# Kernel optimization log

Hardware: AMD Instinct MI355X
Metric: run time of the kernel (lower is better)

## Reference

```python
import jax, jax.numpy as jnp
import numpy as np

B, N, D, C, K = 16, 8192, 128, 64, 4
SEQ_LEN, PRED_LEN = 96, 192
BASE_TEMP = 2.0


def setup_inputs() -> dict:
    key = jax.random.key(0)
    kx, kd = jax.random.split(key)
    x = jax.random.normal(kx, (B, N, D), dtype=jnp.float32)
    # nn.Parameter(torch.randn(C, D)) followed by nn.init.orthogonal_ -> orthonormal rows
    dict_raw = jax.random.normal(kd, (C, D), dtype=jnp.float32)
    qmat, _ = jnp.linalg.qr(dict_raw.T)  # (D, C), orthonormal columns since D >= C
    dictionary = qmat.T  # (C, D) with orthonormal rows
    return {"x": x, "dictionary": dictionary}


def reference(x, dictionary):
    # x: (B, N, D); dictionary: (C, D)
    temp = BASE_TEMP * (1.0 + PRED_LEN / SEQ_LEN)  # seq_len/pred_len branch active
    scores = jnp.einsum('bnd,cd->bnc', x, dictionary)  # (B, N, C)

    # soft assignment q and KL self-training loss against target distribution p (no grad through p)
    logq = jax.nn.log_softmax(scores / temp, axis=-1)
    q = jnp.exp(logq)
    q_flat = q.reshape(-1, C)  # (B*N, C)
    w = q_flat ** 2 / q_flat.sum(axis=0)
    p = jax.lax.stop_gradient(w / w.sum(axis=1, keepdims=True))
    # F.kl_div(log q, p, reduction='batchmean') = sum(p * (log p - log q)) / (B*N)
    kl_loss = jnp.sum(p * (jnp.log(p) - logq.reshape(-1, C))) / (B * N)

    # orthogonality regularizer on dictionary gram matrix
    gram = dictionary @ dictionary.T  # (C, C)
    ortho_loss = jnp.mean((gram - jnp.eye(C, dtype=dictionary.dtype)) ** 2)
    aux_loss = kl_loss * (SEQ_LEN / PRED_LEN) + 0.1 * ortho_loss

    # top-k hard routing: masked softmax over top-k scores == softmax over the top-k values
    topk_vals, topk_idx = jax.lax.top_k(scores, K)  # (B, N, K)
    wk = jax.nn.softmax(topk_vals / temp, axis=-1)  # (B, N, K)
    # gather only the K selected dictionary rows instead of dense (B,N,C,D) expand
    x_common = jnp.einsum('bnk,bnkd->bnd', wk, dictionary[topk_idx])
    x_residual = x - x_common
    return (x_common, x_residual, aux_loss)
```

## Files before the change

### kernel.cpp

```cpp
#include <hip/hip_runtime.h>
#include <math.h>

#define BB 16
#define NN 8192
#define DD 128
#define CC 64
#define ROWS (BB*NN)
#define INV_TEMP (1.0f/6.0f)
#define NEGF (-3.402823e38f)
#define LDSS 132

#define RPB 128
#define CHW 32
#define XST 34

__device__ __forceinline__ unsigned f2bf(float f) {
    unsigned u = __builtin_bit_cast(unsigned, f);
    return (u + 0x7fffu + ((u >> 16) & 1u)) >> 16;
}
__device__ __forceinline__ float bflo(unsigned u) { return __builtin_bit_cast(float, u << 16); }
__device__ __forceinline__ float bfhi(unsigned u) { return __builtin_bit_cast(float, u & 0xffff0000u); }

__global__ __launch_bounds__(256, 4) void k_main(
    const float* __restrict__ x, const float* __restrict__ dict,
    float* __restrict__ xcg, float* __restrict__ xrg,
    unsigned* __restrict__ qg, float* __restrict__ colpart)
{
    __shared__ __align__(16) float bufA[RPB * XST];
    __shared__ float red2[RPB][2];
    __shared__ float colsumA[CC];
    __shared__ __align__(16) float w4s[RPB][4];
    __shared__ __align__(16) int   si4s[RPB][4];

    const int tid   = threadIdx.x;
    const int rloc  = tid & (RPB - 1);
    const int chalf = tid >> 7;
    const int cbase = __builtin_amdgcn_readfirstlane(chalf << 5);
    const int row0  = blockIdx.x * RPB;

    if (tid < CC) colsumA[tid] = 0.f;

    const int sr = tid >> 3;
    const int sj = (tid & 7) * 4;
    const float* xstage = x + (size_t)(row0 + sr) * DD + sj;

    float s[32];
#pragma unroll
    for (int cc = 0; cc < 32; ++cc) s[cc] = 0.f;

    float4 rp[4];
#pragma unroll
    for (int p = 0; p < 4; ++p)
        rp[p] = *(const float4*)(xstage + (size_t)p * 32 * DD);
#pragma unroll
    for (int p = 0; p < 4; ++p) {
        float* dst = &bufA[XST * (sr + 32 * p) + sj];
        *(float2*)dst       = make_float2(rp[p].x, rp[p].y);
        *(float2*)(dst + 2) = make_float2(rp[p].z, rp[p].w);
    }
    __syncthreads();

    for (int ch = 0; ch < 4; ++ch) {
        const int j0 = ch * CHW;
        if (ch < 3) {
#pragma unroll
            for (int p = 0; p < 4; ++p)
                rp[p] = *(const float4*)(xstage + (size_t)p * 32 * DD + (j0 + CHW));
        }
        const float* xrow = &bufA[XST * rloc];
        for (int js = 0; js < CHW; js += 4) {
            const float2 x01 = *(const float2*)(xrow + js);
            const float2 x23 = *(const float2*)(xrow + js + 2);
            const float* dcol = dict + (size_t)cbase * DD + (j0 + js);
#pragma unroll
            for (int cc = 0; cc < 32; ++cc) {
                const float* dp = dcol + cc * DD;
                float acc = s[cc];
                acc = fmaf(x01.x, dp[0], acc);
                acc = fmaf(x01.y, dp[1], acc);
                acc = fmaf(x23.x, dp[2], acc);
                acc = fmaf(x23.y, dp[3], acc);
                s[cc] = acc;
            }
        }
        if (ch < 3) {
            __syncthreads();
#pragma unroll
            for (int p = 0; p < 4; ++p) {
                float* dst = &bufA[XST * (sr + 32 * p) + sj];
                *(float2*)dst       = make_float2(rp[p].x, rp[p].y);
                *(float2*)(dst + 2) = make_float2(rp[p].z, rp[p].w);
            }
            __syncthreads();
        }
    }

    float lm = s[0];
#pragma unroll
    for (int cc = 1; cc < 32; ++cc) lm = fmaxf(lm, s[cc]);
    red2[rloc][chalf] = lm;
    __syncthreads();
    const float mg = fmaxf(red2[rloc][0], red2[rloc][1]);
    __syncthreads();

    float tv[4]; int ti[4];
    {
        float best = NEGF; int bi = 0;
#pragma unroll
        for (int cc = 0; cc < 32; ++cc) { if (s[cc] > best) { best = s[cc]; bi = cc; } }
        tv[0] = best; ti[0] = bi;
    }
    {
        float best = NEGF; int bi = 0;
#pragma unroll
        for (int cc = 0; cc < 32; ++cc) {
            const float v = (cc == ti[0]) ? NEGF : s[cc];
            if (v > best) { best = v; bi = cc; }
        }
        tv[1] = best; ti[1] = bi;
    }
    {
        float best = NEGF; int bi = 0;
#pragma unroll
        for (int cc = 0; cc < 32; ++cc) {
            const float v = (cc == ti[0] || cc == ti[1]) ? NEGF : s[cc];
            if (v > best) { best = v; bi = cc; }
        }
        tv[2] = best; ti[2] = bi;
    }
    {
        float best = NEGF; int bi = 0;
#pragma unroll
        for (int cc = 0; cc < 32; ++cc) {
            const float v = (cc == ti[0] || cc == ti[1] || cc == ti[2]) ? NEGF : s[cc];
            if (v > best) { best = v; bi = cc; }
        }
        tv[3] = best; ti[3] = bi;
    }

    float lz = 0.f;
#pragma unroll
    for (int cc = 0; cc < 32; ++cc) {
        const float e = __expf((s[cc] - mg) * INV_TEMP);
        s[cc] = e; lz += e;
    }
    red2[rloc][chalf] = lz;
    __syncthreads();
    const float rZ = 1.f / (red2[rloc][0] + red2[rloc][1]);
#pragma unroll
    for (int cc = 0; cc < 32; ++cc) s[cc] *= rZ;

    float* t4v = bufA;
    int*   t4i = (int*)(bufA + 1024);
    {
        const int b4 = (rloc * 2 + chalf) * 4;
#pragma unroll
        for (int k = 0; k < 4; ++k) { t4v[b4 + k] = tv[k]; t4i[b4 + k] = cbase + ti[k]; }
    }
    __syncthreads();
    float cv[8]; int ci[8];
#pragma unroll
    for (int h = 0; h < 2; ++h) {
#pragma unroll
        for (int k = 0; k < 4; ++k) {
            cv[h * 4 + k] = t4v[(rloc * 2 + h) * 4 + k];
            ci[h * 4 + k] = t4i[(rloc * 2 + h) * 4 + k];
        }
    }
    __syncthreads();

    int rank[8];
#pragma unroll
    for (int j = 0; j < 8; ++j) rank[j] = 0;
#pragma unroll
    for (int j = 0; j < 8; ++j) {
#pragma unroll
        for (int k = 0; k < 8; ++k) {
            if (k == j) continue;
            const bool kg = (cv[k] > cv[j]) || (cv[k] == cv[j] && ci[k] < ci[j]);
            rank[j] += kg ? 1 : 0;
        }
    }
    float sv[4]; int si[4];
#pragma unroll
    for (int t2 = 0; t2 < 4; ++t2) { sv[t2] = NEGF; si[t2] = 0; }
#pragma unroll
    for (int j = 0; j < 8; ++j) {
#pragma unroll
        for (int t2 = 0; t2 < 4; ++t2) {
            const bool sel = (rank[j] == t2);
            sv[t2] = sel ? cv[j] : sv[t2];
            si[t2] = sel ? ci[j] : si[t2];
        }
    }
    const float e1 = __expf((sv[1] - sv[0]) * INV_TEMP);
    const float e2 = __expf((sv[2] - sv[0]) * INV_TEMP);
    const float e3 = __expf((sv[3] - sv[0]) * INV_TEMP);
    const float rZ4 = 1.f / (1.f + e1 + e2 + e3);
    const float w0 = rZ4, w1 = e1 * rZ4, w2 = e2 * rZ4, w3 = e3 * rZ4;

    if (chalf == 0) {
        *(float4*)&w4s[rloc][0] = make_float4(w0, w1, w2, w3);
        *(int4*)&si4s[rloc][0]  = make_int4(si[0], si[1], si[2], si[3]);
    }

    {
        unsigned* qs = (unsigned*)bufA;
        const int base = XST * rloc + 16 * chalf;
#pragma unroll
        for (int k2 = 0; k2 < 16; k2 += 2) {
            uint2 w;
            w.x = (f2bf(s[2 * k2 + 1]) << 16) | f2bf(s[2 * k2 + 0]);
            w.y = (f2bf(s[2 * k2 + 3]) << 16) | f2bf(s[2 * k2 + 2]);
            *(uint2*)&qs[base + k2] = w;
        }
        __syncthreads();
        unsigned* qdst = qg + (size_t)blockIdx.x * (RPB * 32);
#pragma unroll
        for (int k4 = 0; k4 < 4; ++k4) {
            const int gd  = k4 * 1024 + tid * 4;
            const int row = gd >> 5, kk = gd & 31;
            const uint2 a = *(const uint2*)&qs[XST * row + kk];
            const uint2 b = *(const uint2*)&qs[XST * row + kk + 2];
            uint4 o; o.x = a.x; o.y = a.y; o.z = b.x; o.w = b.y;
            *(uint4*)&qdst[gd] = o;
        }
        const int cp  = tid & 31;
        const int rr0 = (tid >> 5) * 16;
        float c0 = 0.f, c1 = 0.f;
#pragma unroll
        for (int rr = 0; rr < 16; ++rr) {
            const unsigned u = qs[XST * (rr0 + rr) + cp];
            c0 += bflo(u); c1 += bfhi(u);
        }
        atomicAdd(&colsumA[2 * cp + 0], c0);
        atomicAdd(&colsumA[2 * cp + 1], c1);
    }
    __syncthreads();
    if (tid < CC) colpart[blockIdx.x * CC + tid] = colsumA[tid];

#pragma unroll 2
    for (int it = 0; it < 16; ++it) {
        const int gd  = it * 1024 + tid * 4;
        const int row = gd >> 7;
        const int dd  = gd & 127;
        const float4 wv = *(const float4*)&w4s[row][0];
        const int4  iv  = *(const int4*)&si4s[row][0];
        const size_t go = (size_t)(row0 + row) * DD + dd;
        const float4 xv = *(const float4*)(x + go);
        const float4 d0 = *(const float4*)(dict + (size_t)iv.x * DD + dd);
        const float4 d1 = *(const float4*)(dict + (size_t)iv.y * DD + dd);
        const float4 d2 = *(const float4*)(dict + (size_t)iv.z * DD + dd);
        const float4 d3 = *(const float4*)(dict + (size_t)iv.w * DD + dd);
        float4 c4, r4;
        c4.x = fmaf(wv.w, d3.x, fmaf(wv.z, d2.x, fmaf(wv.y, d1.x, wv.x * d0.x)));
        c4.y = fmaf(wv.w, d3.y, fmaf(wv.z, d2.y, fmaf(wv.y, d1.y, wv.x * d0.y)));
        c4.z = fmaf(wv.w, d3.z, fmaf(wv.z, d2.z, fmaf(wv.y, d1.z, wv.x * d0.z)));
        c4.w = fmaf(wv.w, d3.w, fmaf(wv.z, d2.w, fmaf(wv.y, d1.w, wv.x * d0.w)));
        r4.x = xv.x - c4.x; r4.y = xv.y - c4.y;
        r4.z = xv.z - c4.z; r4.w = xv.w - c4.w;
        *(float4*)(xcg + go) = c4;
        *(float4*)(xrg + go) = r4;
    }
}

__global__ void k_colsum(const float* __restrict__ colpart, float* __restrict__ colsum)
{
    const int tid = threadIdx.x;
    const int c   = tid & 63;
    const int seg = blockIdx.x * 4 + (tid >> 6);
    float v = 0.f;
#pragma unroll
    for (int b = 0; b < 16; ++b)
        v += colpart[(seg * 16 + b) * 64 + c];
    atomicAdd(&colsum[c], v);
}

__global__ __launch_bounds__(256, 2) void k_kl(
    const unsigned* __restrict__ qg, const float* __restrict__ colsum,
    float* __restrict__ klacc)
{
    __shared__ __align__(8) unsigned qs[256 * XST];
    __shared__ float rF[CC], lF[CC];
    __shared__ float kred[4];
    const int tid = threadIdx.x;
    if (tid < CC) { const float F = colsum[tid]; rF[tid] = 1.f / F; lF[tid] = __logf(F); }
    const unsigned* qb = qg + (size_t)blockIdx.x * 8192;
#pragma unroll
    for (int g = 0; g < 8; ++g) {
        const int gd = g * 1024 + tid * 4;
        const uint4 v = *(const uint4*)(qb + gd);
        const int row = gd >> 5, kk = gd & 31;
        *(uint2*)&qs[XST * row + kk]     = make_uint2(v.x, v.y);
        *(uint2*)&qs[XST * row + kk + 2] = make_uint2(v.z, v.w);
    }
    __syncthreads();
    const unsigned* qr = &qs[XST * tid];
    unsigned u[32];
#pragma unroll
    for (int k = 0; k < 32; k += 2) {
        const uint2 t2 = *(const uint2*)&qr[k];
        u[k] = t2.x; u[k + 1] = t2.y;
    }
    float S = 0.f;
#pragma unroll
    for (int k = 0; k < 32; ++k) {
        const float f0 = bflo(u[k]), f1 = bfhi(u[k]);
        S = fmaf(f0 * f0, rF[2 * k], S);
        S = fmaf(f1 * f1, rF[2 * k + 1], S);
    }
    const float rS = 1.f / S;
    const float lS = __logf(S);
    float acc = 0.f;
#pragma unroll
    for (int k = 0; k < 32; ++k) {
        const float f0 = bflo(u[k]), f1 = bfhi(u[k]);
        const float p0 = f0 * f0 * rF[2 * k] * rS;
        const float p1 = f1 * f1 * rF[2 * k + 1] * rS;
        acc += p0 * (__logf(f0) - lF[2 * k] - lS);
        acc += p1 * (__logf(f1) - lF[2 * k + 1] - lS);
    }
#pragma unroll
    for (int off = 32; off > 0; off >>= 1) acc += __shfl_down(acc, off, 64);
    if ((tid & 63) == 0) kred[tid >> 6] = acc;
    __syncthreads();
    if (tid == 0) atomicAdd(klacc, kred[0] + kred[1] + kred[2] + kred[3]);
}

__global__ __launch_bounds__(256) void k_ortho(
    const float* __restrict__ dict, float* __restrict__ oacc)
{
    __shared__ __align__(16) float dlds[CC * LDSS];
    const int tid = threadIdx.x;
    for (int idx = tid; idx < CC * DD; idx += 256)
        dlds[(idx >> 7) * LDSS + (idx & 127)] = dict[idx];
    __syncthreads();

    const int e = blockIdx.x * 256 + tid;
    const int i = e >> 6, jj = e & 63;
    const float* di = &dlds[i * LDSS];
    const float* dj = &dlds[jj * LDSS];
    float g = 0.f;
#pragma unroll 8
    for (int d = 0; d < DD; d += 4) {
        const float4 a = *(const float4*)(di + d);
        const float4 b = *(const float4*)(dj + d);
        g += a.x * b.x + a.y * b.y + a.z * b.z + a.w * b.w;
    }
    const float diff = g - ((i == jj) ? 1.f : 0.f);
    float v = diff * diff;
#pragma unroll
    for (int off = 32; off > 0; off >>= 1)
        v += __shfl_down(v, off, 64);
    if ((tid & 63) == 0) atomicAdd(oacc, v);
}

__global__ void k_final(const float* __restrict__ klacc,
                        const float* __restrict__ oacc,
                        float* __restrict__ out_scalar)
{
    out_scalar[0] = 0.5f * (klacc[0] / (float)ROWS) + 0.1f * (oacc[0] / 4096.f);
}

extern "C" void kernel_launch(void* const* d_in, const int* in_sizes, int n_in,
                              void* d_out, int out_size, void* d_ws, size_t ws_size,
                              hipStream_t stream)
{
    const float* x    = (const float*)d_in[0];
    const float* dict = (const float*)d_in[1];
    float* out = (float*)d_out;
    float* xcg = out;
    float* xrg = out + (size_t)ROWS * DD;
    float* aux = out + 2 * (size_t)ROWS * DD;

    float* ws      = (float*)d_ws;
    float* colsum  = ws;
    float* klacc   = ws + 64;
    float* oacc    = ws + 65;
    float* colpart = ws + 256;
    unsigned* qbuf = (unsigned*)(ws + 256 + 1024 * 64);

    hipMemsetAsync(d_ws, 0, 1024, stream);

    k_main  <<<ROWS / RPB, 256, 0, stream>>>(x, dict, xcg, xrg, qbuf, colpart);
    k_colsum<<<16,         256, 0, stream>>>(colpart, colsum);
    k_kl    <<<ROWS / 256, 256, 0, stream>>>(qbuf, colsum, klacc);
    k_ortho <<<16,         256, 0, stream>>>(dict, oacc);
    k_final <<<1,          1,   0, stream>>>(klacc, oacc, aux);
}
```

Measured before the change: 276.3 us.

## Fuse pipeline into one cooperative kernel with grid syncs, keep q in registers

Replaces the five-kernel sequence with a single cooperative-launch kernel that uses grid-wide syncs to compute column sums, the ortho loss, the KL loss and the final aux scalar. The soft-assignment probabilities stay in registers instead of being written as bf16 to global memory and reread by a separate KL kernel. Launch overhead and the q round trip go away. In exchange it needs all 1024 blocks co-resident (4 per CU) and pays three grid barriers, and it falls back to the old multi-kernel path if the cooperative launch fails.

```diff
diff --git a/kernel.cpp b/kernel.cpp
--- a/kernel.cpp
+++ b/kernel.cpp
@@ -1,5 +1,8 @@
 #include <hip/hip_runtime.h>
+#include <hip/hip_cooperative_groups.h>
 #include <math.h>
+
+namespace cg = cooperative_groups;
 
 #define BB 16
 #define NN 8192
@@ -21,10 +24,12 @@
 __device__ __forceinline__ float bflo(unsigned u) { return __builtin_bit_cast(float, u << 16); }
 __device__ __forceinline__ float bfhi(unsigned u) { return __builtin_bit_cast(float, u & 0xffff0000u); }
 
-__global__ __launch_bounds__(256, 4) void k_main(
+__global__ __launch_bounds__(256, 4) void k_fused(
     const float* __restrict__ x, const float* __restrict__ dict,
     float* __restrict__ xcg, float* __restrict__ xrg,
-    unsigned* __restrict__ qg, float* __restrict__ colpart)
+    float* __restrict__ colpart, float* __restrict__ colsum,
+    float* __restrict__ klacc, float* __restrict__ oacc,
+    float* __restrict__ aux)
 {
     __shared__ __align__(16) float bufA[RPB * XST];
     __shared__ float red2[RPB][2];
@@ -32,12 +37,16 @@
     __shared__ __align__(16) float w4s[RPB][4];
     __shared__ __align__(16) int   si4s[RPB][4];
 
+    cg::grid_group gg = cg::this_grid();
+
     const int tid   = threadIdx.x;
     const int rloc  = tid & (RPB - 1);
     const int chalf = tid >> 7;
     const int cbase = __builtin_amdgcn_readfirstlane(chalf << 5);
-    const int row0  = blockIdx.x * RPB;
-
+    const int bid   = blockIdx.x;
+    const int row0  = bid * RPB;
+
+    if (bid == 0 && tid == 0) { klacc[0] = 0.f; oacc[0] = 0.f; }
     if (tid < CC) colsumA[tid] = 0.f;
 
     const int sr = tid >> 3;
@@ -215,16 +224,6 @@
             *(uint2*)&qs[base + k2] = w;
         }
         __syncthreads();
-        unsigned* qdst = qg + (size_t)blockIdx.x * (RPB * 32);
-#pragma unroll
-        for (int k4 = 0; k4 < 4; ++k4) {
-            const int gd  = k4 * 1024 + tid * 4;
-            const int row = gd >> 5, kk = gd & 31;
-            const uint2 a = *(const uint2*)&qs[XST * row + kk];
-            const uint2 b = *(const uint2*)&qs[XST * row + kk + 2];
-            uint4 o; o.x = a.x; o.y = a.y; o.z = b.x; o.w = b.y;
-            *(uint4*)&qdst[gd] = o;
-        }
         const int cp  = tid & 31;
         const int rr0 = (tid >> 5) * 16;
         float c0 = 0.f, c1 = 0.f;
@@ -237,7 +236,75 @@
         atomicAdd(&colsumA[2 * cp + 1], c1);
     }
     __syncthreads();
-    if (tid < CC) colpart[blockIdx.x * CC + tid] = colsumA[tid];
+    if (tid < CC) colpart[bid * CC + tid] = colsumA[tid];
+
+    gg.sync();
+
+    if (bid == 0) {
+        const int c = tid & 63, qt = tid >> 6;
+        float v = 0.f;
+#pragma unroll 8
+        for (int i = 0; i < 256; ++i)
+            v += colpart[(size_t)(((qt << 8) + i) * 64 + c)];
+        float* cred = bufA;
+        cred[tid] = v;
+        __syncthreads();
+        if (tid < CC)
+            colsum[tid] = cred[tid] + cred[tid + 64] + cred[tid + 128] + cred[tid + 192];
+    } else if (bid >= 64 && bid < 80) {
+        const int e = (bid - 64) * 256 + tid;
+        const int i = e >> 6, jj = e & 63;
+        const float* di = dict + (size_t)i * DD;
+        const float* dj = dict + (size_t)jj * DD;
+        float g = 0.f;
+#pragma unroll 8
+        for (int d = 0; d < DD; d += 4) {
+            const float4 a = *(const float4*)(di + d);
+            const float4 b = *(const float4*)(dj + d);
+            g += a.x * b.x + a.y * b.y + a.z * b.z + a.w * b.w;
+        }
+        const float diff = g - ((i == jj) ? 1.f : 0.f);
+        float v = diff * diff;
+#pragma unroll
+        for (int off = 32; off > 0; off >>= 1)
+            v += __shfl_down(v, off, 64);
+        if ((tid & 63) == 0) atomicAdd(oacc, v);
+    }
+
+    gg.sync();
+
+    {
+        float* rF   = bufA;
+        float* lF   = bufA + 64;
+        float* kred = bufA + 128;
+        if (tid < CC) { const float F = colsum[tid]; rF[tid] = 1.f / F; lF[tid] = __logf(F); }
+        __syncthreads();
+        float Sh = 0.f;
+#pragma unroll
+        for (int cc = 0; cc < 32; ++cc) Sh = fmaf(s[cc] * s[cc], rF[cbase + cc], Sh);
+        red2[rloc][chalf] = Sh;
+        __syncthreads();
+        const float Sr = red2[rloc][0] + red2[rloc][1];
+        const float rS = 1.f / Sr;
+        const float lS = __logf(Sr);
+        float acc = 0.f;
+#pragma unroll
+        for (int cc = 0; cc < 32; ++cc) {
+            const float q = s[cc];
+            const float p = q * q * rF[cbase + cc] * rS;
+            acc += p * (__logf(q) - lF[cbase + cc] - lS);
+        }
+#pragma unroll
+        for (int off = 32; off > 0; off >>= 1) acc += __shfl_down(acc, off, 64);
+        if ((tid & 63) == 0) kred[tid >> 6] = acc;
+        __syncthreads();
+        if (tid == 0) atomicAdd(klacc, kred[0] + kred[1] + kred[2] + kred[3]);
+    }
+
+    gg.sync();
+
+    if (bid == 0 && tid == 0)
+        aux[0] = 0.5f * (klacc[0] / (float)ROWS) + 0.1f * (oacc[0] / 4096.f);
 
 #pragma unroll 2
     for (int it = 0; it < 16; ++it) {
@@ -264,6 +331,249 @@
     }
 }
 
+__global__ __launch_bounds__(256, 4) void k_main(
+    const float* __restrict__ x, const float* __restrict__ dict,
+    float* __restrict__ xcg, float* __restrict__ xrg,
+    unsigned* __restrict__ qg, float* __restrict__ colpart)
+{
+    __shared__ __align__(16) float bufA[RPB * XST];
+    __shared__ float red2[RPB][2];
+    __shared__ float colsumA[CC];
+    __shared__ __align__(16) float w4s[RPB][4];
+    __shared__ __align__(16) int   si4s[RPB][4];
+
+    const int tid   = threadIdx.x;
+    const int rloc  = tid & (RPB - 1);
+    const int chalf = tid >> 7;
+    const int cbase = __builtin_amdgcn_readfirstlane(chalf << 5);
+    const int row0  = blockIdx.x * RPB;
+
+    if (tid < CC) colsumA[tid] = 0.f;
+
+    const int sr = tid >> 3;
+    const int sj = (tid & 7) * 4;
+    const float* xstage = x + (size_t)(row0 + sr) * DD + sj;
+
+    float s[32];
+#pragma unroll
+    for (int cc = 0; cc < 32; ++cc) s[cc] = 0.f;
+
+    float4 rp[4];
+#pragma unroll
+    for (int p = 0; p < 4; ++p)
+        rp[p] = *(const float4*)(xstage + (size_t)p * 32 * DD);
+#pragma unroll
+    for (int p = 0; p < 4; ++p) {
+        float* dst = &bufA[XST * (sr + 32 * p) + sj];
+        *(float2*)dst       = make_float2(rp[p].x, rp[p].y);
+        *(float2*)(dst + 2) = make_float2(rp[p].z, rp[p].w);
+    }
+    __syncthreads();
+
+    for (int ch = 0; ch < 4; ++ch) {
+        const int j0 = ch * CHW;
+        if (ch < 3) {
+#pragma unroll
+            for (int p = 0; p < 4; ++p)
+                rp[p] = *(const float4*)(xstage + (size_t)p * 32 * DD + (j0 + CHW));
+        }
+        const float* xrow = &bufA[XST * rloc];
+        for (int js = 0; js < CHW; js += 4) {
+            const float2 x01 = *(const float2*)(xrow + js);
+            const float2 x23 = *(const float2*)(xrow + js + 2);
+            const float* dcol = dict + (size_t)cbase * DD + (j0 + js);
+#pragma unroll
+            for (int cc = 0; cc < 32; ++cc) {
+                const float* dp = dcol + cc * DD;
+                float acc = s[cc];
+                acc = fmaf(x01.x, dp[0], acc);
+                acc = fmaf(x01.y, dp[1], acc);
+                acc = fmaf(x23.x, dp[2], acc);
+                acc = fmaf(x23.y, dp[3], acc);
+                s[cc] = acc;
+            }
+        }
+        if (ch < 3) {
+            __syncthreads();
+#pragma unroll
+            for (int p = 0; p < 4; ++p) {
+                float* dst = &bufA[XST * (sr + 32 * p) + sj];
+                *(float2*)dst       = make_float2(rp[p].x, rp[p].y);
+                *(float2*)(dst + 2) = make_float2(rp[p].z, rp[p].w);
+            }
+            __syncthreads();
+        }
+    }
+
+    float lm = s[0];
+#pragma unroll
+    for (int cc = 1; cc < 32; ++cc) lm = fmaxf(lm, s[cc]);
+    red2[rloc][chalf] = lm;
+    __syncthreads();
+    const float mg = fmaxf(red2[rloc][0], red2[rloc][1]);
+    __syncthreads();
+
+    float tv[4]; int ti[4];
+    {
+        float best = NEGF; int bi = 0;
+#pragma unroll
+        for (int cc = 0; cc < 32; ++cc) { if (s[cc] > best) { best = s[cc]; bi = cc; } }
+        tv[0] = best; ti[0] = bi;
+    }
+    {
+        float best = NEGF; int bi = 0;
+#pragma unroll
+        for (int cc = 0; cc < 32; ++cc) {
+            const float v = (cc == ti[0]) ? NEGF : s[cc];
+            if (v > best) { best = v; bi = cc; }
+        }
+        tv[1] = best; ti[1] = bi;
+    }
+    {
+        float best = NEGF; int bi = 0;
+#pragma unroll
+        for (int cc = 0; cc < 32; ++cc) {
+            const float v = (cc == ti[0] || cc == ti[1]) ? NEGF : s[cc];
+            if (v > best) { best = v; bi = cc; }
+        }
+        tv[2] = best; ti[2] = bi;
+    }
+    {
+        float best = NEGF; int bi = 0;
+#pragma unroll
+        for (int cc = 0; cc < 32; ++cc) {
+            const float v = (cc == ti[0] || cc == ti[1] || cc == ti[2]) ? NEGF : s[cc];
+            if (v > best) { best = v; bi = cc; }
+        }
+        tv[3] = best; ti[3] = bi;
+    }
+
+    float lz = 0.f;
+#pragma unroll
+    for (int cc = 0; cc < 32; ++cc) {
+        const float e = __expf((s[cc] - mg) * INV_TEMP);
+        s[cc] = e; lz += e;
+    }
+    red2[rloc][chalf] = lz;
+    __syncthreads();
+    const float rZ = 1.f / (red2[rloc][0] + red2[rloc][1]);
+#pragma unroll
+    for (int cc = 0; cc < 32; ++cc) s[cc] *= rZ;
+
+    float* t4v = bufA;
+    int*   t4i = (int*)(bufA + 1024);
+    {
+        const int b4 = (rloc * 2 + chalf) * 4;
+#pragma unroll
+        for (int k = 0; k < 4; ++k) { t4v[b4 + k] = tv[k]; t4i[b4 + k] = cbase + ti[k]; }
+    }
+    __syncthreads();
+    float cv[8]; int ci[8];
+#pragma unroll
+    for (int h = 0; h < 2; ++h) {
+#pragma unroll
+        for (int k = 0; k < 4; ++k) {
+            cv[h * 4 + k] = t4v[(rloc * 2 + h) * 4 + k];
+            ci[h * 4 + k] = t4i[(rloc * 2 + h) * 4 + k];
+        }
+    }
+    __syncthreads();
+
+    int rank[8];
+#pragma unroll
+    for (int j = 0; j < 8; ++j) rank[j] = 0;
+#pragma unroll
+    for (int j = 0; j < 8; ++j) {
+#pragma unroll
+        for (int k = 0; k < 8; ++k) {
+            if (k == j) continue;
+            const bool kg = (cv[k] > cv[j]) || (cv[k] == cv[j] && ci[k] < ci[j]);
+            rank[j] += kg ? 1 : 0;
+        }
+    }
+    float sv[4]; int si[4];
+#pragma unroll
+    for (int t2 = 0; t2 < 4; ++t2) { sv[t2] = NEGF; si[t2] = 0; }
+#pragma unroll
+    for (int j = 0; j < 8; ++j) {
+#pragma unroll
+        for (int t2 = 0; t2 < 4; ++t2) {
+            const bool sel = (rank[j] == t2);
+            sv[t2] = sel ? cv[j] : sv[t2];
+            si[t2] = sel ? ci[j] : si[t2];
+        }
+    }
+    const float e1 = __expf((sv[1] - sv[0]) * INV_TEMP);
+    const float e2 = __expf((sv[2] - sv[0]) * INV_TEMP);
+    const float e3 = __expf((sv[3] - sv[0]) * INV_TEMP);
+    const float rZ4 = 1.f / (1.f + e1 + e2 + e3);
+    const float w0 = rZ4, w1 = e1 * rZ4, w2 = e2 * rZ4, w3 = e3 * rZ4;
+
+    if (chalf == 0) {
+        *(float4*)&w4s[rloc][0] = make_float4(w0, w1, w2, w3);
+        *(int4*)&si4s[rloc][0]  = make_int4(si[0], si[1], si[2], si[3]);
+    }
+
+    {
+        unsigned* qs = (unsigned*)bufA;
+        const int base = XST * rloc + 16 * chalf;
+#pragma unroll
+        for (int k2 = 0; k2 < 16; k2 += 2) {
+            uint2 w;
+            w.x = (f2bf(s[2 * k2 + 1]) << 16) | f2bf(s[2 * k2 + 0]);
+            w.y = (f2bf(s[2 * k2 + 3]) << 16) | f2bf(s[2 * k2 + 2]);
+            *(uint2*)&qs[base + k2] = w;
+        }
+        __syncthreads();
+        unsigned* qdst = qg + (size_t)blockIdx.x * (RPB * 32);
+#pragma unroll
+        for (int k4 = 0; k4 < 4; ++k4) {
+            const int gd  = k4 * 1024 + tid * 4;
+            const int row = gd >> 5, kk = gd & 31;
+            const uint2 a = *(const uint2*)&qs[XST * row + kk];
+            const uint2 b = *(const uint2*)&qs[XST * row + kk + 2];
+            uint4 o; o.x = a.x; o.y = a.y; o.z = b.x; o.w = b.y;
+            *(uint4*)&qdst[gd] = o;
+        }
+        const int cp  = tid & 31;
+        const int rr0 = (tid >> 5) * 16;
+        float c0 = 0.f, c1 = 0.f;
+#pragma unroll
+        for (int rr = 0; rr < 16; ++rr) {
+            const unsigned u = qs[XST * (rr0 + rr) + cp];
+            c0 += bflo(u); c1 += bfhi(u);
+        }
+        atomicAdd(&colsumA[2 * cp + 0], c0);
+        atomicAdd(&colsumA[2 * cp + 1], c1);
+    }
+    __syncthreads();
+    if (tid < CC) colpart[blockIdx.x * CC + tid] = colsumA[tid];
+
+#pragma unroll 2
+    for (int it = 0; it < 16; ++it) {
+        const int gd  = it * 1024 + tid * 4;
+        const int row = gd >> 7;
+        const int dd  = gd & 127;
+        const float4 wv = *(const float4*)&w4s[row][0];
+        const int4  iv  = *(const int4*)&si4s[row][0];
+        const size_t go = (size_t)(row0 + row) * DD + dd;
+        const float4 xv = *(const float4*)(x + go);
+        const float4 d0 = *(const float4*)(dict + (size_t)iv.x * DD + dd);
+        const float4 d1 = *(const float4*)(dict + (size_t)iv.y * DD + dd);
+        const float4 d2 = *(const float4*)(dict + (size_t)iv.z * DD + dd);
+        const float4 d3 = *(const float4*)(dict + (size_t)iv.w * DD + dd);
+        float4 c4, r4;
+        c4.x = fmaf(wv.w, d3.x, fmaf(wv.z, d2.x, fmaf(wv.y, d1.x, wv.x * d0.x)));
+        c4.y = fmaf(wv.w, d3.y, fmaf(wv.z, d2.y, fmaf(wv.y, d1.y, wv.x * d0.y)));
+        c4.z = fmaf(wv.w, d3.z, fmaf(wv.z, d2.z, fmaf(wv.y, d1.z, wv.x * d0.z)));
+        c4.w = fmaf(wv.w, d3.w, fmaf(wv.z, d2.w, fmaf(wv.y, d1.w, wv.x * d0.w)));
+        r4.x = xv.x - c4.x; r4.y = xv.y - c4.y;
+        r4.z = xv.z - c4.z; r4.w = xv.w - c4.w;
+        *(float4*)(xcg + go) = c4;
+        *(float4*)(xrg + go) = r4;
+    }
+}
+
 __global__ void k_colsum(const float* __restrict__ colpart, float* __restrict__ colsum)
 {
     const int tid = threadIdx.x;
@@ -380,11 +690,26 @@
     float* colpart = ws + 256;
     unsigned* qbuf = (unsigned*)(ws + 256 + 1024 * 64);
 
-    hipMemsetAsync(d_ws, 0, 1024, stream);
-
-    k_main  <<<ROWS / RPB, 256, 0, stream>>>(x, dict, xcg, xrg, qbuf, colpart);
-    k_colsum<<<16,         256, 0, stream>>>(colpart, colsum);
-    k_kl    <<<ROWS / 256, 256, 0, stream>>>(qbuf, colsum, klacc);
-    k_ortho <<<16,         256, 0, stream>>>(dict, oacc);
-    k_final <<<1,          1,   0, stream>>>(klacc, oacc, aux);
+    void* kargs[9];
+    kargs[0] = (void*)&x;
+    kargs[1] = (void*)&dict;
+    kargs[2] = (void*)&xcg;
+    kargs[3] = (void*)&xrg;
+    kargs[4] = (void*)&colpart;
+    kargs[5] = (void*)&colsum;
+    kargs[6] = (void*)&klacc;
+    kargs[7] = (void*)&oacc;
+    kargs[8] = (void*)&aux;
+
+    hipError_t rc = hipLaunchCooperativeKernel((const void*)k_fused,
+                                               dim3(ROWS / RPB), dim3(256),
+                                               kargs, 0, stream);
+    if (rc != hipSuccess) {
+        hipMemsetAsync(d_ws, 0, 1024, stream);
+        k_main  <<<ROWS / RPB, 256, 0, stream>>>(x, dict, xcg, xrg, qbuf, colpart);
+        k_colsum<<<16,         256, 0, stream>>>(colpart, colsum);
+        k_kl    <<<ROWS / 256, 256, 0, stream>>>(qbuf, colsum, klacc);
+        k_ortho <<<16,         256, 0, stream>>>(dict, oacc);
+        k_final <<<1,          1,   0, stream>>>(klacc, oacc, aux);
+    }
 }
```

Result: slower. 527.9 us (+91.1%).

## Fuse all stages into one kernel with a grid-wide flag barrier

Applied to the files above, without the earlier changes.

Merges the colsum, KL, ortho and final kernels into the main kernel. The last block to finish reduces the per-block column partials and raises a flag. Every block spins on that flag after writing its outputs, then computes the KL term from the q values still held in registers. This removes the bf16 q buffer write and re-read and four extra launches, and the ortho work moves onto 16 of the blocks. In exchange it relies on all 1024 blocks being resident at once; if they are not, the spin-wait deadlocks.

```diff
diff --git a/kernel.cpp b/kernel.cpp
--- a/kernel.cpp
+++ b/kernel.cpp
@@ -8,11 +8,11 @@
 #define ROWS (BB*NN)
 #define INV_TEMP (1.0f/6.0f)
 #define NEGF (-3.402823e38f)
-#define LDSS 132
 
 #define RPB 128
 #define CHW 32
 #define XST 34
+#define GRID (ROWS / RPB)
 
 __device__ __forceinline__ unsigned f2bf(float f) {
     unsigned u = __builtin_bit_cast(unsigned, f);
@@ -21,22 +21,27 @@
 __device__ __forceinline__ float bflo(unsigned u) { return __builtin_bit_cast(float, u << 16); }
 __device__ __forceinline__ float bfhi(unsigned u) { return __builtin_bit_cast(float, u & 0xffff0000u); }
 
-__global__ __launch_bounds__(256, 4) void k_main(
+__global__ __launch_bounds__(256, 4) void k_all(
     const float* __restrict__ x, const float* __restrict__ dict,
     float* __restrict__ xcg, float* __restrict__ xrg,
-    unsigned* __restrict__ qg, float* __restrict__ colpart)
+    float* __restrict__ colpart, float* __restrict__ colsum,
+    float* __restrict__ klacc, float* __restrict__ oacc,
+    unsigned* __restrict__ cnt1, unsigned* __restrict__ flag,
+    unsigned* __restrict__ cnt2, float* __restrict__ aux)
 {
     __shared__ __align__(16) float bufA[RPB * XST];
     __shared__ float red2[RPB][2];
     __shared__ float colsumA[CC];
     __shared__ __align__(16) float w4s[RPB][4];
     __shared__ __align__(16) int   si4s[RPB][4];
+    __shared__ int lastA;
 
     const int tid   = threadIdx.x;
     const int rloc  = tid & (RPB - 1);
     const int chalf = tid >> 7;
     const int cbase = __builtin_amdgcn_readfirstlane(chalf << 5);
-    const int row0  = blockIdx.x * RPB;
+    const int bid   = blockIdx.x;
+    const int row0  = bid * RPB;
 
     if (tid < CC) colsumA[tid] = 0.f;
 
@@ -215,16 +220,6 @@
             *(uint2*)&qs[base + k2] = w;
         }
         __syncthreads();
-        unsigned* qdst = qg + (size_t)blockIdx.x * (RPB * 32);
-#pragma unroll
-        for (int k4 = 0; k4 < 4; ++k4) {
-            const int gd  = k4 * 1024 + tid * 4;
-            const int row = gd >> 5, kk = gd & 31;
-            const uint2 a = *(const uint2*)&qs[XST * row + kk];
-            const uint2 b = *(const uint2*)&qs[XST * row + kk + 2];
-            uint4 o; o.x = a.x; o.y = a.y; o.z = b.x; o.w = b.y;
-            *(uint4*)&qdst[gd] = o;
-        }
         const int cp  = tid & 31;
         const int rr0 = (tid >> 5) * 16;
         float c0 = 0.f, c1 = 0.f;
@@ -237,7 +232,52 @@
         atomicAdd(&colsumA[2 * cp + 1], c1);
     }
     __syncthreads();
-    if (tid < CC) colpart[blockIdx.x * CC + tid] = colsumA[tid];
+    if (tid < CC) colpart[bid * CC + tid] = colsumA[tid];
+
+    if (bid >= 64 && bid < 80) {
+        const int e = (bid - 64) * 256 + tid;
+        const int i = e >> 6, jj = e & 63;
+        const float* di = dict + (size_t)i * DD;
+        const float* dj = dict + (size_t)jj * DD;
+        float g = 0.f;
+#pragma unroll 8
+        for (int d = 0; d < DD; d += 4) {
+            const float4 a = *(const float4*)(di + d);
+            const float4 b = *(const float4*)(dj + d);
+            g += a.x * b.x + a.y * b.y + a.z * b.z + a.w * b.w;
+        }
+        const float diff = g - ((i == jj) ? 1.f : 0.f);
+        float v = diff * diff;
+#pragma unroll
+        for (int off = 32; off > 0; off >>= 1)
+            v += __shfl_down(v, off, 64);
+        if ((tid & 63) == 0) atomicAdd(oacc, v);
+    }
+
+    __syncthreads();
+    if (tid == 0) {
+        const unsigned prev = __hip_atomic_fetch_add(
+            cnt1, 1u, __ATOMIC_ACQ_REL, __HIP_MEMORY_SCOPE_AGENT);
+        lastA = (prev == (unsigned)(GRID - 1)) ? 1 : 0;
+    }
+    __syncthreads();
+    if (lastA) {
+        const int c = tid & 63, qt = tid >> 6;
+        float v = 0.f;
+#pragma unroll 8
+        for (int i = 0; i < 256; ++i)
+            v += colpart[(size_t)(((qt << 8) + i) * 64 + c)];
+        float* cred = bufA;
+        cred[tid] = v;
+        __syncthreads();
+        if (tid < CC)
+            __hip_atomic_store(&colsum[tid],
+                cred[tid] + cred[tid + 64] + cred[tid + 128] + cred[tid + 192],
+                __ATOMIC_RELAXED, __HIP_MEMORY_SCOPE_AGENT);
+        __syncthreads();
+        if (tid == 0)
+            __hip_atomic_store(flag, 1u, __ATOMIC_RELEASE, __HIP_MEMORY_SCOPE_AGENT);
+    }
 
 #pragma unroll 2
     for (int it = 0; it < 16; ++it) {
@@ -262,104 +302,55 @@
         *(float4*)(xcg + go) = c4;
         *(float4*)(xrg + go) = r4;
     }
-}
-
-__global__ void k_colsum(const float* __restrict__ colpart, float* __restrict__ colsum)
-{
-    const int tid = threadIdx.x;
-    const int c   = tid & 63;
-    const int seg = blockIdx.x * 4 + (tid >> 6);
-    float v = 0.f;
-#pragma unroll
-    for (int b = 0; b < 16; ++b)
-        v += colpart[(seg * 16 + b) * 64 + c];
-    atomicAdd(&colsum[c], v);
-}
-
-__global__ __launch_bounds__(256, 2) void k_kl(
-    const unsigned* __restrict__ qg, const float* __restrict__ colsum,
-    float* __restrict__ klacc)
-{
-    __shared__ __align__(8) unsigned qs[256 * XST];
-    __shared__ float rF[CC], lF[CC];
-    __shared__ float kred[4];
-    const int tid = threadIdx.x;
-    if (tid < CC) { const float F = colsum[tid]; rF[tid] = 1.f / F; lF[tid] = __logf(F); }
-    const unsigned* qb = qg + (size_t)blockIdx.x * 8192;
-#pragma unroll
-    for (int g = 0; g < 8; ++g) {
-        const int gd = g * 1024 + tid * 4;
-        const uint4 v = *(const uint4*)(qb + gd);
-        const int row = gd >> 5, kk = gd & 31;
-        *(uint2*)&qs[XST * row + kk]     = make_uint2(v.x, v.y);
-        *(uint2*)&qs[XST * row + kk + 2] = make_uint2(v.z, v.w);
-    }
-    __syncthreads();
-    const unsigned* qr = &qs[XST * tid];
-    unsigned u[32];
-#pragma unroll
-    for (int k = 0; k < 32; k += 2) {
-        const uint2 t2 = *(const uint2*)&qr[k];
-        u[k] = t2.x; u[k + 1] = t2.y;
-    }
-    float S = 0.f;
-#pragma unroll
-    for (int k = 0; k < 32; ++k) {
-        const float f0 = bflo(u[k]), f1 = bfhi(u[k]);
-        S = fmaf(f0 * f0, rF[2 * k], S);
-        S = fmaf(f1 * f1, rF[2 * k + 1], S);
-    }
-    const float rS = 1.f / S;
-    const float lS = __logf(S);
-    float acc = 0.f;
-#pragma unroll
-    for (int k = 0; k < 32; ++k) {
-        const float f0 = bflo(u[k]), f1 = bfhi(u[k]);
-        const float p0 = f0 * f0 * rF[2 * k] * rS;
-        const float p1 = f1 * f1 * rF[2 * k + 1] * rS;
-        acc += p0 * (__logf(f0) - lF[2 * k] - lS);
-        acc += p1 * (__logf(f1) - lF[2 * k + 1] - lS);
-    }
-#pragma unroll
-    for (int off = 32; off > 0; off >>= 1) acc += __shfl_down(acc, off, 64);
-    if ((tid & 63) == 0) kred[tid >> 6] = acc;
-    __syncthreads();
-    if (tid == 0) atomicAdd(klacc, kred[0] + kred[1] + kred[2] + kred[3]);
-}
-
-__global__ __launch_bounds__(256) void k_ortho(
-    const float* __restrict__ dict, float* __restrict__ oacc)
-{
-    __shared__ __align__(16) float dlds[CC * LDSS];
-    const int tid = threadIdx.x;
-    for (int idx = tid; idx < CC * DD; idx += 256)
-        dlds[(idx >> 7) * LDSS + (idx & 127)] = dict[idx];
-    __syncthreads();
-
-    const int e = blockIdx.x * 256 + tid;
-    const int i = e >> 6, jj = e & 63;
-    const float* di = &dlds[i * LDSS];
-    const float* dj = &dlds[jj * LDSS];
-    float g = 0.f;
-#pragma unroll 8
-    for (int d = 0; d < DD; d += 4) {
-        const float4 a = *(const float4*)(di + d);
-        const float4 b = *(const float4*)(dj + d);
-        g += a.x * b.x + a.y * b.y + a.z * b.z + a.w * b.w;
-    }
-    const float diff = g - ((i == jj) ? 1.f : 0.f);
-    float v = diff * diff;
-#pragma unroll
-    for (int off = 32; off > 0; off >>= 1)
-        v += __shfl_down(v, off, 64);
-    if ((tid & 63) == 0) atomicAdd(oacc, v);
-}
-
-__global__ void k_final(const float* __restrict__ klacc,
-                        const float* __restrict__ oacc,
-                        float* __restrict__ out_scalar)
-{
-    out_scalar[0] = 0.5f * (klacc[0] / (float)ROWS) + 0.1f * (oacc[0] / 4096.f);
+
+    if (tid == 0) {
+        while (__hip_atomic_load(flag, __ATOMIC_ACQUIRE, __HIP_MEMORY_SCOPE_AGENT) == 0u)
+            __builtin_amdgcn_s_sleep(8);
+    }
+    __syncthreads();
+
+    {
+        float* rF   = bufA;
+        float* lF   = bufA + 64;
+        float* kred = bufA + 128;
+        if (tid < CC) {
+            const float F = __hip_atomic_load(&colsum[tid],
+                __ATOMIC_RELAXED, __HIP_MEMORY_SCOPE_AGENT);
+            rF[tid] = 1.f / F; lF[tid] = __logf(F);
+        }
+        __syncthreads();
+        float Sh = 0.f;
+#pragma unroll
+        for (int cc = 0; cc < 32; ++cc) Sh = fmaf(s[cc] * s[cc], rF[cbase + cc], Sh);
+        red2[rloc][chalf] = Sh;
+        __syncthreads();
+        const float Sr = red2[rloc][0] + red2[rloc][1];
+        const float rS = 1.f / Sr;
+        const float lS = __logf(Sr);
+        float acc = 0.f;
+#pragma unroll
+        for (int cc = 0; cc < 32; ++cc) {
+            const float q = s[cc];
+            const float p = q * q * rF[cbase + cc] * rS;
+            acc += p * (__logf(q) - lF[cbase + cc] - lS);
+        }
+#pragma unroll
+        for (int off = 32; off > 0; off >>= 1) acc += __shfl_down(acc, off, 64);
+        if ((tid & 63) == 0) kred[tid >> 6] = acc;
+        __syncthreads();
+        if (tid == 0) {
+            atomicAdd(klacc, kred[0] + kred[1] + kred[2] + kred[3]);
+            const unsigned prev = __hip_atomic_fetch_add(
+                cnt2, 1u, __ATOMIC_ACQ_REL, __HIP_MEMORY_SCOPE_AGENT);
+            if (prev == (unsigned)(GRID - 1)) {
+                const float kt = __hip_atomic_load(klacc,
+                    __ATOMIC_RELAXED, __HIP_MEMORY_SCOPE_AGENT);
+                const float ot = __hip_atomic_load(oacc,
+                    __ATOMIC_RELAXED, __HIP_MEMORY_SCOPE_AGENT);
+                aux[0] = 0.5f * (kt / (float)ROWS) + 0.1f * (ot / 4096.f);
+            }
+        }
+    }
 }
 
 extern "C" void kernel_launch(void* const* d_in, const int* in_sizes, int n_in,
@@ -373,18 +364,17 @@
     float* xrg = out + (size_t)ROWS * DD;
     float* aux = out + 2 * (size_t)ROWS * DD;
 
-    float* ws      = (float*)d_ws;
-    float* colsum  = ws;
-    float* klacc   = ws + 64;
-    float* oacc    = ws + 65;
-    float* colpart = ws + 256;
-    unsigned* qbuf = (unsigned*)(ws + 256 + 1024 * 64);
+    float* ws       = (float*)d_ws;
+    float* colsum   = ws;
+    float* klacc    = ws + 64;
+    float* oacc     = ws + 65;
+    unsigned* cnt1  = (unsigned*)(ws + 66);
+    unsigned* flag  = (unsigned*)(ws + 67);
+    unsigned* cnt2  = (unsigned*)(ws + 68);
+    float* colpart  = ws + 256;
 
     hipMemsetAsync(d_ws, 0, 1024, stream);
 
-    k_main  <<<ROWS / RPB, 256, 0, stream>>>(x, dict, xcg, xrg, qbuf, colpart);
-    k_colsum<<<16,         256, 0, stream>>>(colpart, colsum);
-    k_kl    <<<ROWS / 256, 256, 0, stream>>>(qbuf, colsum, klacc);
-    k_ortho <<<16,         256, 0, stream>>>(dict, oacc);
-    k_final <<<1,          1,   0, stream>>>(klacc, oacc, aux);
+    k_all<<<GRID, 256, 0, stream>>>(x, dict, xcg, xrg, colpart, colsum,
+                                    klacc, oacc, cnt1, flag, cnt2, aux);
 }
```

Measured after the change: 388.6 us. 1.41x slower.

## Split channels four ways per row, halve rows per block, merge tail kernels

Applied to the files above, without the earlier changes.

The main kernel now handles 64 rows per block with four 16-channel groups per row instead of 128 rows with two 32-channel halves. This halves per-thread score registers and allows a higher occupancy target. The top-4 merge now draws on 16 candidates through transposed LDS arrays. The colsum and ortho kernels are fused into one tail launch, and the final scalar is written by the last KL block through an atomic counter, which removes two launches. The cost is twice as many main-kernel blocks, more partial colsums to reduce, and a larger candidate merge per row.

```diff
diff --git a/kernel.cpp b/kernel.cpp
--- a/kernel.cpp
+++ b/kernel.cpp
@@ -8,11 +8,11 @@
 #define ROWS (BB*NN)
 #define INV_TEMP (1.0f/6.0f)
 #define NEGF (-3.402823e38f)
-#define LDSS 132
-
-#define RPB 128
+
+#define RPB 64
 #define CHW 32
 #define XST 34
+#define GRIDM (ROWS / RPB)
 
 __device__ __forceinline__ unsigned f2bf(float f) {
     unsigned u = __builtin_bit_cast(unsigned, f);
@@ -21,21 +21,23 @@
 __device__ __forceinline__ float bflo(unsigned u) { return __builtin_bit_cast(float, u << 16); }
 __device__ __forceinline__ float bfhi(unsigned u) { return __builtin_bit_cast(float, u & 0xffff0000u); }
 
-__global__ __launch_bounds__(256, 4) void k_main(
+__global__ __launch_bounds__(256, 8) void k_main(
     const float* __restrict__ x, const float* __restrict__ dict,
     float* __restrict__ xcg, float* __restrict__ xrg,
     unsigned* __restrict__ qg, float* __restrict__ colpart)
 {
     __shared__ __align__(16) float bufA[RPB * XST];
-    __shared__ float red2[RPB][2];
+    __shared__ __align__(16) float t4v[16][RPB];
+    __shared__ __align__(16) int   t4i[16][RPB];
+    __shared__ float red4[RPB][4];
     __shared__ float colsumA[CC];
     __shared__ __align__(16) float w4s[RPB][4];
     __shared__ __align__(16) int   si4s[RPB][4];
 
     const int tid   = threadIdx.x;
     const int rloc  = tid & (RPB - 1);
-    const int chalf = tid >> 7;
-    const int cbase = __builtin_amdgcn_readfirstlane(chalf << 5);
+    const int qh    = tid >> 6;
+    const int cbase = __builtin_amdgcn_readfirstlane(qh << 4);
     const int row0  = blockIdx.x * RPB;
 
     if (tid < CC) colsumA[tid] = 0.f;
@@ -44,16 +46,16 @@
     const int sj = (tid & 7) * 4;
     const float* xstage = x + (size_t)(row0 + sr) * DD + sj;
 
-    float s[32];
-#pragma unroll
-    for (int cc = 0; cc < 32; ++cc) s[cc] = 0.f;
-
-    float4 rp[4];
-#pragma unroll
-    for (int p = 0; p < 4; ++p)
+    float s[16];
+#pragma unroll
+    for (int cc = 0; cc < 16; ++cc) s[cc] = 0.f;
+
+    float4 rp[2];
+#pragma unroll
+    for (int p = 0; p < 2; ++p)
         rp[p] = *(const float4*)(xstage + (size_t)p * 32 * DD);
 #pragma unroll
-    for (int p = 0; p < 4; ++p) {
+    for (int p = 0; p < 2; ++p) {
         float* dst = &bufA[XST * (sr + 32 * p) + sj];
         *(float2*)dst       = make_float2(rp[p].x, rp[p].y);
         *(float2*)(dst + 2) = make_float2(rp[p].z, rp[p].w);
@@ -64,7 +66,7 @@
         const int j0 = ch * CHW;
         if (ch < 3) {
 #pragma unroll
-            for (int p = 0; p < 4; ++p)
+            for (int p = 0; p < 2; ++p)
                 rp[p] = *(const float4*)(xstage + (size_t)p * 32 * DD + (j0 + CHW));
         }
         const float* xrow = &bufA[XST * rloc];
@@ -73,7 +75,7 @@
             const float2 x23 = *(const float2*)(xrow + js + 2);
             const float* dcol = dict + (size_t)cbase * DD + (j0 + js);
 #pragma unroll
-            for (int cc = 0; cc < 32; ++cc) {
+            for (int cc = 0; cc < 16; ++cc) {
                 const float* dp = dcol + cc * DD;
                 float acc = s[cc];
                 acc = fmaf(x01.x, dp[0], acc);
@@ -86,7 +88,7 @@
         if (ch < 3) {
             __syncthreads();
 #pragma unroll
-            for (int p = 0; p < 4; ++p) {
+            for (int p = 0; p < 2; ++p) {
                 float* dst = &bufA[XST * (sr + 32 * p) + sj];
                 *(float2*)dst       = make_float2(rp[p].x, rp[p].y);
                 *(float2*)(dst + 2) = make_float2(rp[p].z, rp[p].w);
@@ -97,23 +99,23 @@
 
     float lm = s[0];
 #pragma unroll
-    for (int cc = 1; cc < 32; ++cc) lm = fmaxf(lm, s[cc]);
-    red2[rloc][chalf] = lm;
-    __syncthreads();
-    const float mg = fmaxf(red2[rloc][0], red2[rloc][1]);
-    __syncthreads();
+    for (int cc = 1; cc < 16; ++cc) lm = fmaxf(lm, s[cc]);
+    red4[rloc][qh] = lm;
+    __syncthreads();
+    const float mg = fmaxf(fmaxf(red4[rloc][0], red4[rloc][1]),
+                           fmaxf(red4[rloc][2], red4[rloc][3]));
 
     float tv[4]; int ti[4];
     {
         float best = NEGF; int bi = 0;
 #pragma unroll
-        for (int cc = 0; cc < 32; ++cc) { if (s[cc] > best) { best = s[cc]; bi = cc; } }
+        for (int cc = 0; cc < 16; ++cc) { if (s[cc] > best) { best = s[cc]; bi = cc; } }
         tv[0] = best; ti[0] = bi;
     }
     {
         float best = NEGF; int bi = 0;
 #pragma unroll
-        for (int cc = 0; cc < 32; ++cc) {
+        for (int cc = 0; cc < 16; ++cc) {
             const float v = (cc == ti[0]) ? NEGF : s[cc];
             if (v > best) { best = v; bi = cc; }
         }
@@ -122,7 +124,7 @@
     {
         float best = NEGF; int bi = 0;
 #pragma unroll
-        for (int cc = 0; cc < 32; ++cc) {
+        for (int cc = 0; cc < 16; ++cc) {
             const float v = (cc == ti[0] || cc == ti[1]) ? NEGF : s[cc];
             if (v > best) { best = v; bi = cc; }
         }
@@ -131,7 +133,7 @@
     {
         float best = NEGF; int bi = 0;
 #pragma unroll
-        for (int cc = 0; cc < 32; ++cc) {
+        for (int cc = 0; cc < 16; ++cc) {
             const float v = (cc == ti[0] || cc == ti[1] || cc == ti[2]) ? NEGF : s[cc];
             if (v > best) { best = v; bi = cc; }
         }
@@ -140,84 +142,53 @@
 
     float lz = 0.f;
 #pragma unroll
-    for (int cc = 0; cc < 32; ++cc) {
+    for (int cc = 0; cc < 16; ++cc) {
         const float e = __expf((s[cc] - mg) * INV_TEMP);
         s[cc] = e; lz += e;
     }
-    red2[rloc][chalf] = lz;
-    __syncthreads();
-    const float rZ = 1.f / (red2[rloc][0] + red2[rloc][1]);
-#pragma unroll
-    for (int cc = 0; cc < 32; ++cc) s[cc] *= rZ;
-
-    float* t4v = bufA;
-    int*   t4i = (int*)(bufA + 1024);
-    {
-        const int b4 = (rloc * 2 + chalf) * 4;
-#pragma unroll
-        for (int k = 0; k < 4; ++k) { t4v[b4 + k] = tv[k]; t4i[b4 + k] = cbase + ti[k]; }
-    }
-    __syncthreads();
-    float cv[8]; int ci[8];
-#pragma unroll
-    for (int h = 0; h < 2; ++h) {
-#pragma unroll
-        for (int k = 0; k < 4; ++k) {
-            cv[h * 4 + k] = t4v[(rloc * 2 + h) * 4 + k];
-            ci[h * 4 + k] = t4i[(rloc * 2 + h) * 4 + k];
-        }
-    }
-    __syncthreads();
-
-    int rank[8];
-#pragma unroll
-    for (int j = 0; j < 8; ++j) rank[j] = 0;
-#pragma unroll
-    for (int j = 0; j < 8; ++j) {
-#pragma unroll
-        for (int k = 0; k < 8; ++k) {
-            if (k == j) continue;
-            const bool kg = (cv[k] > cv[j]) || (cv[k] == cv[j] && ci[k] < ci[j]);
-            rank[j] += kg ? 1 : 0;
-        }
-    }
-    float sv[4]; int si[4];
-#pragma unroll
-    for (int t2 = 0; t2 < 4; ++t2) { sv[t2] = NEGF; si[t2] = 0; }
-#pragma unroll
-    for (int j = 0; j < 8; ++j) {
-#pragma unroll
-        for (int t2 = 0; t2 < 4; ++t2) {
-            const bool sel = (rank[j] == t2);
-            sv[t2] = sel ? cv[j] : sv[t2];
-            si[t2] = sel ? ci[j] : si[t2];
-        }
-    }
-    const float e1 = __expf((sv[1] - sv[0]) * INV_TEMP);
-    const float e2 = __expf((sv[2] - sv[0]) * INV_TEMP);
-    const float e3 = __expf((sv[3] - sv[0]) * INV_TEMP);
-    const float rZ4 = 1.f / (1.f + e1 + e2 + e3);
-    const float w0 = rZ4, w1 = e1 * rZ4, w2 = e2 * rZ4, w3 = e3 * rZ4;
-
-    if (chalf == 0) {
-        *(float4*)&w4s[rloc][0] = make_float4(w0, w1, w2, w3);
-        *(int4*)&si4s[rloc][0]  = make_int4(si[0], si[1], si[2], si[3]);
-    }
-
-    {
-        unsigned* qs = (unsigned*)bufA;
-        const int base = XST * rloc + 16 * chalf;
-#pragma unroll
-        for (int k2 = 0; k2 < 16; k2 += 2) {
+    __syncthreads();
+    red4[rloc][qh] = lz;
+    __syncthreads();
+    const float rZ = 1.f / (red4[rloc][0] + red4[rloc][1] + red4[rloc][2] + red4[rloc][3]);
+#pragma unroll
+    for (int cc = 0; cc < 16; ++cc) s[cc] *= rZ;
+
+#pragma unroll
+    for (int k = 0; k < 4; ++k) {
+        t4v[qh * 4 + k][rloc] = tv[k];
+        t4i[qh * 4 + k][rloc] = cbase + ti[k];
+    }
+
+    unsigned* qs = (unsigned*)bufA;
+    {
+        const int base = XST * rloc + 8 * qh;
+#pragma unroll
+        for (int k2 = 0; k2 < 8; k2 += 2) {
             uint2 w;
             w.x = (f2bf(s[2 * k2 + 1]) << 16) | f2bf(s[2 * k2 + 0]);
             w.y = (f2bf(s[2 * k2 + 3]) << 16) | f2bf(s[2 * k2 + 2]);
             *(uint2*)&qs[base + k2] = w;
         }
-        __syncthreads();
+    }
+    __syncthreads();
+
+    {
+        const int cp  = tid & 31;
+        const int rr0 = (tid >> 5) * 8;
+        float c0 = 0.f, c1 = 0.f;
+#pragma unroll
+        for (int rr = 0; rr < 8; ++rr) {
+            const unsigned u = qs[XST * (rr0 + rr) + cp];
+            c0 += bflo(u); c1 += bfhi(u);
+        }
+        atomicAdd(&colsumA[2 * cp + 0], c0);
+        atomicAdd(&colsumA[2 * cp + 1], c1);
+    }
+
+    {
         unsigned* qdst = qg + (size_t)blockIdx.x * (RPB * 32);
 #pragma unroll
-        for (int k4 = 0; k4 < 4; ++k4) {
+        for (int k4 = 0; k4 < 2; ++k4) {
             const int gd  = k4 * 1024 + tid * 4;
             const int row = gd >> 5, kk = gd & 31;
             const uint2 a = *(const uint2*)&qs[XST * row + kk];
@@ -225,22 +196,43 @@
             uint4 o; o.x = a.x; o.y = a.y; o.z = b.x; o.w = b.y;
             *(uint4*)&qdst[gd] = o;
         }
-        const int cp  = tid & 31;
-        const int rr0 = (tid >> 5) * 16;
-        float c0 = 0.f, c1 = 0.f;
-#pragma unroll
-        for (int rr = 0; rr < 16; ++rr) {
-            const unsigned u = qs[XST * (rr0 + rr) + cp];
-            c0 += bflo(u); c1 += bfhi(u);
-        }
-        atomicAdd(&colsumA[2 * cp + 0], c0);
-        atomicAdd(&colsumA[2 * cp + 1], c1);
+    }
+
+    {
+        float cv[16]; int ci[16];
+#pragma unroll
+        for (int m = 0; m < 16; ++m) { cv[m] = t4v[m][rloc]; ci[m] = t4i[m][rloc]; }
+        float sv[4]; int si[4];
+#pragma unroll
+        for (int t = 0; t < 4; ++t) {
+            float best = NEGF; int bi = 1 << 30;
+#pragma unroll
+            for (int m = 0; m < 16; ++m) {
+                bool used = false;
+#pragma unroll
+                for (int u2 = 0; u2 < 3; ++u2)
+                    if (u2 < t) used = used || (ci[m] == si[u2]);
+                const bool better = !used &&
+                    (cv[m] > best || (cv[m] == best && ci[m] < bi));
+                best = better ? cv[m] : best;
+                bi   = better ? ci[m] : bi;
+            }
+            sv[t] = best; si[t] = bi;
+        }
+        const float e1 = __expf((sv[1] - sv[0]) * INV_TEMP);
+        const float e2 = __expf((sv[2] - sv[0]) * INV_TEMP);
+        const float e3 = __expf((sv[3] - sv[0]) * INV_TEMP);
+        const float rZ4 = 1.f / (1.f + e1 + e2 + e3);
+        if (qh == 0) {
+            *(float4*)&w4s[rloc][0] = make_float4(rZ4, e1 * rZ4, e2 * rZ4, e3 * rZ4);
+            *(int4*)&si4s[rloc][0]  = make_int4(si[0], si[1], si[2], si[3]);
+        }
     }
     __syncthreads();
     if (tid < CC) colpart[blockIdx.x * CC + tid] = colsumA[tid];
 
 #pragma unroll 2
-    for (int it = 0; it < 16; ++it) {
+    for (int it = 0; it < 8; ++it) {
         const int gd  = it * 1024 + tid * 4;
         const int row = gd >> 7;
         const int dd  = gd & 127;
@@ -264,21 +256,44 @@
     }
 }
 
-__global__ void k_colsum(const float* __restrict__ colpart, float* __restrict__ colsum)
+__global__ __launch_bounds__(256) void k_tail(
+    const float* __restrict__ colpart, float* __restrict__ colsum,
+    const float* __restrict__ dict, float* __restrict__ oacc)
 {
     const int tid = threadIdx.x;
-    const int c   = tid & 63;
-    const int seg = blockIdx.x * 4 + (tid >> 6);
-    float v = 0.f;
-#pragma unroll
-    for (int b = 0; b < 16; ++b)
-        v += colpart[(seg * 16 + b) * 64 + c];
-    atomicAdd(&colsum[c], v);
+    if (blockIdx.x < 16) {
+        const int c   = tid & 63;
+        const int seg = blockIdx.x * 4 + (tid >> 6);
+        float v = 0.f;
+#pragma unroll 8
+        for (int b = 0; b < 32; ++b)
+            v += colpart[(size_t)((seg * 32 + b) * 64 + c)];
+        atomicAdd(&colsum[c], v);
+    } else {
+        const int e = (blockIdx.x - 16) * 256 + tid;
+        const int i = e >> 6, jj = e & 63;
+        const float* di = dict + (size_t)i * DD;
+        const float* dj = dict + (size_t)jj * DD;
+        float g = 0.f;
+#pragma unroll 8
+        for (int d = 0; d < DD; d += 4) {
+            const float4 a = *(const float4*)(di + d);
+            const float4 b = *(const float4*)(dj + d);
+            g += a.x * b.x + a.y * b.y + a.z * b.z + a.w * b.w;
+        }
+        const float diff = g - ((i == jj) ? 1.f : 0.f);
+        float v = diff * diff;
+#pragma unroll
+        for (int off = 32; off > 0; off >>= 1)
+            v += __shfl_down(v, off, 64);
+        if ((tid & 63) == 0) atomicAdd(oacc, v);
+    }
 }
 
 __global__ __launch_bounds__(256, 2) void k_kl(
     const unsigned* __restrict__ qg, const float* __restrict__ colsum,
-    float* __restrict__ klacc)
+    float* __restrict__ klacc, const float* __restrict__ oacc,
+    unsigned* __restrict__ cnt, float* __restrict__ aux)
 {
     __shared__ __align__(8) unsigned qs[256 * XST];
     __shared__ float rF[CC], lF[CC];
@@ -324,42 +339,18 @@
     for (int off = 32; off > 0; off >>= 1) acc += __shfl_down(acc, off, 64);
     if ((tid & 63) == 0) kred[tid >> 6] = acc;
     __syncthreads();
-    if (tid == 0) atomicAdd(klacc, kred[0] + kred[1] + kred[2] + kred[3]);
-}
-
-__global__ __launch_bounds__(256) void k_ortho(
-    const float* __restrict__ dict, float* __restrict__ oacc)
-{
-    __shared__ __align__(16) float dlds[CC * LDSS];
-    const int tid = threadIdx.x;
-    for (int idx = tid; idx < CC * DD; idx += 256)
-        dlds[(idx >> 7) * LDSS + (idx & 127)] = dict[idx];
-    __syncthreads();
-
-    const int e = blockIdx.x * 256 + tid;
-    const int i = e >> 6, jj = e & 63;
-    const float* di = &dlds[i * LDSS];
-    const float* dj = &dlds[jj * LDSS];
-    float g = 0.f;
-#pragma unroll 8
-    for (int d = 0; d < DD; d += 4) {
-        const float4 a = *(const float4*)(di + d);
-        const float4 b = *(const float4*)(dj + d);
-        g += a.x * b.x + a.y * b.y + a.z * b.z + a.w * b.w;
-    }
-    const float diff = g - ((i == jj) ? 1.f : 0.f);
-    float v = diff * diff;
-#pragma unroll
-    for (int off = 32; off > 0; off >>= 1)
-        v += __shfl_down(v, off, 64);
-    if ((tid & 63) == 0) atomicAdd(oacc, v);
-}
-
-__global__ void k_final(const float* __restrict__ klacc,
-                        const float* __restrict__ oacc,
-                        float* __restrict__ out_scalar)
-{
-    out_scalar[0] = 0.5f * (klacc[0] / (float)ROWS) + 0.1f * (oacc[0] / 4096.f);
+    if (tid == 0) {
+        atomicAdd(klacc, kred[0] + kred[1] + kred[2] + kred[3]);
+        const unsigned prev = __hip_atomic_fetch_add(
+            cnt, 1u, __ATOMIC_ACQ_REL, __HIP_MEMORY_SCOPE_AGENT);
+        if (prev == (unsigned)(ROWS / 256 - 1)) {
+            const float kt = __hip_atomic_load(klacc,
+                __ATOMIC_RELAXED, __HIP_MEMORY_SCOPE_AGENT);
+            const float ot = __hip_atomic_load((float*)oacc,
+                __ATOMIC_RELAXED, __HIP_MEMORY_SCOPE_AGENT);
+            aux[0] = 0.5f * (kt / (float)ROWS) + 0.1f * (ot / 4096.f);
+        }
+    }
 }
 
 extern "C" void kernel_launch(void* const* d_in, const int* in_sizes, int n_in,
@@ -373,18 +364,17 @@
     float* xrg = out + (size_t)ROWS * DD;
     float* aux = out + 2 * (size_t)ROWS * DD;
 
-    float* ws      = (float*)d_ws;
-    float* colsum  = ws;
-    float* klacc   = ws + 64;
-    float* oacc    = ws + 65;
-    float* colpart = ws + 256;
-    unsigned* qbuf = (unsigned*)(ws + 256 + 1024 * 64);
+    float* ws       = (float*)d_ws;
+    float* colsum   = ws;
+    float* klacc    = ws + 64;
+    float* oacc     = ws + 65;
+    unsigned* cnt   = (unsigned*)(ws + 66);
+    float* colpart  = ws + 256;
+    unsigned* qbuf  = (unsigned*)(ws + 256 + GRIDM * CC);
 
     hipMemsetAsync(d_ws, 0, 1024, stream);
 
-    k_main  <<<ROWS / RPB, 256, 0, stream>>>(x, dict, xcg, xrg, qbuf, colpart);
-    k_colsum<<<16,         256, 0, stream>>>(colpart, colsum);
-    k_kl    <<<ROWS / 256, 256, 0, stream>>>(qbuf, colsum, klacc);
-    k_ortho <<<16,         256, 0, stream>>>(dict, oacc);
-    k_final <<<1,          1,   0, stream>>>(klacc, oacc, aux);
-}
+    k_main<<<GRIDM,      256, 0, stream>>>(x, dict, xcg, xrg, qbuf, colpart);
+    k_tail<<<32,         256, 0, stream>>>(colpart, colsum, dict, oacc);
+    k_kl  <<<ROWS / 256, 256, 0, stream>>>(qbuf, colsum, klacc, oacc, cnt, aux);
+}
```

Result: no change. 280.5 us (+1.5%).
